# Kernel tuning notes

Measured on AMD Instinct MI355X. Metric: run time of the kernel, lower is better.

## Reference

```python
import jax, jax.numpy as jnp
import numpy as np
import math

K = 8  # n_prototypes
SQRT_2_OVER_PI = 0.7978845608028654  # sqrt(2/pi)
EPS = 1e-12  # torch F.normalize eps


def _gelu(x):
    # tanh-approx GELU, matching the module's _gelu
    return 0.5 * x * (1.0 + jnp.tanh(SQRT_2_OVER_PI * (x + 0.044715 * x * x * x)))


def _l2norm(x, axis=-1):
    n = jnp.linalg.norm(x, axis=axis, keepdims=True)
    return x / jnp.maximum(n, EPS)


def setup_inputs() -> dict:
    key = jax.random.key(0)
    k1, k2 = jax.random.split(key)
    B, T, D = 8, 2048, 2048
    x = jax.random.normal(k1, (B, T, D), dtype=jnp.float32)
    # prototype bank as it exists after initialization: unit-norm rows
    protos = _l2norm(jax.random.normal(k2, (K, D), dtype=jnp.float32))
    log_tau = jnp.asarray(math.log(2.0), dtype=jnp.float32)
    log_gamma = jnp.asarray(math.log(2.0), dtype=jnp.float32)
    log_blend = jnp.asarray(math.log(0.3 / 0.7), dtype=jnp.float32)
    return {"x": x, "protos": protos, "log_tau": log_tau,
            "log_gamma": log_gamma, "log_blend": log_blend}


def reference(x, protos, log_tau, log_gamma, log_blend):
    # steady-state (self._ready == True) forward path
    tau = jnp.exp(log_tau)
    gamma = jnp.exp(log_gamma)
    alpha = jax.nn.sigmoid(log_blend)

    out = _gelu(x)                                  # [B,T,D]
    out_norm = _l2norm(out)                         # [B,T,D]
    proto_norm = _l2norm(protos)                    # [K,D]
    sims = jnp.einsum('btd,kd->btk', out_norm, proto_norm)  # [B,T,K]
    soft_max_sim = (jax.nn.logsumexp(sims * tau, axis=-1) / tau
                    - jnp.log(jnp.float32(K)) / tau)         # [B,T]
    novelty = jnp.exp(-gamma * soft_max_sim)
    gate = 1.0 - alpha + alpha * novelty            # [B,T]
    return out * gate[..., None]
```

## Files before the change

### kernel.cpp

```cpp
#include <hip/hip_runtime.h>
#include <math.h>

#define DDIM 2048
#define KP 8
#define BLOCK 256

typedef float f4 __attribute__((ext_vector_type(4)));

#if __has_builtin(__builtin_amdgcn_fdot2_f32_bf16)
#define HAVE_DOT2 1
typedef __bf16 bf2 __attribute__((ext_vector_type(2)));
#else
#define HAVE_DOT2 0
#endif

#if __has_builtin(__builtin_amdgcn_update_dpp)
#define HAVE_DPP 1
#else
#define HAVE_DPP 0
#endif

__device__ __forceinline__ unsigned short f32_to_bf16_rne(float f) {
    unsigned u = __float_as_uint(f);
    unsigned r = u + 0x7FFFu + ((u >> 16) & 1u);
    return (unsigned short)(r >> 16);
}

__device__ __forceinline__ f4 gelu_f4(f4 x) {
    f4 x2 = x * x;
    f4 inner = x * (x2 * 0.044715f + 1.0f);
    f4 t = inner * -1.5957691216057308f;
    f4 e;
    e.x = __expf(t.x); e.y = __expf(t.y);
    e.z = __expf(t.z); e.w = __expf(t.w);
    f4 den = e + 1.0f;
    f4 r;
    r.x = __builtin_amdgcn_rcpf(den.x); r.y = __builtin_amdgcn_rcpf(den.y);
    r.z = __builtin_amdgcn_rcpf(den.z); r.w = __builtin_amdgcn_rcpf(den.w);
    return x * r;
}

__device__ __forceinline__ float wave_reduce_add(float v) {
#pragma unroll
    for (int m = 32; m >= 1; m >>= 1) v += __shfl_xor(v, m, 64);
    return v;
}

#if HAVE_DPP
template <int CTRL>
__device__ __forceinline__ float dpp_add(float v) {
    int t = __builtin_amdgcn_update_dpp(0, __builtin_bit_cast(int, v),
                                        CTRL, 0xf, 0xf, true);
    return v + __builtin_bit_cast(float, t);
}
__device__ __forceinline__ float wave_sum_dpp_lane63(float v) {
    v = dpp_add<0x111>(v);
    v = dpp_add<0x112>(v);
    v = dpp_add<0x114>(v);
    v = dpp_add<0x118>(v);
    v = dpp_add<0x142>(v);
    v = dpp_add<0x143>(v);
    return v;
}
#endif

__global__ void proto_prep_kernel(const float* __restrict__ protos,
                                  unsigned short* __restrict__ pb,
                                  float* __restrict__ inv_pn) {
    const int k = blockIdx.x;
    const int tid = threadIdx.x;
    const float* p = protos + k * DDIM;
    float ss = 0.0f;
#pragma unroll
    for (int i = 0; i < 2; ++i) {
        int idx = tid + i * 256;
        f4 a = reinterpret_cast<const f4*>(p)[idx];
        ushort4 u;
        u.x = f32_to_bf16_rne(a.x); u.y = f32_to_bf16_rne(a.y);
        u.z = f32_to_bf16_rne(a.z); u.w = f32_to_bf16_rne(a.w);
        float q;
        q = __uint_as_float((unsigned)u.x << 16); ss += q * q;
        q = __uint_as_float((unsigned)u.y << 16); ss += q * q;
        q = __uint_as_float((unsigned)u.z << 16); ss += q * q;
        q = __uint_as_float((unsigned)u.w << 16); ss += q * q;
        *reinterpret_cast<ushort4*>(&pb[(size_t)k * DDIM + idx * 4]) = u;
    }
    ss = wave_reduce_add(ss);
    __shared__ float red[4];
    const int wave = tid >> 6, lane = tid & 63;
    if (lane == 0) red[wave] = ss;
    __syncthreads();
    if (tid == 0)
        inv_pn[k] = 1.0f / fmaxf(sqrtf(red[0] + red[1] + red[2] + red[3]), 1e-12f);
}

__global__ __launch_bounds__(BLOCK)
void fused_row_kernel(const float* __restrict__ x,
                      const unsigned short* __restrict__ pb,
                      const float* __restrict__ lt,
                      const float* __restrict__ lg,
                      const float* __restrict__ lb,
                      const float* __restrict__ inv_pn,
                      float* __restrict__ out, int nrows) {
    alignas(16) __shared__ float red[2][18][4];

    const int tid = threadIdx.x;
    const int lane = tid & 63;
    const int wave = tid >> 6;

    const float tau = __expf(lt[0]);
    const float gamma = __expf(lg[0]);
    const float alpha = 1.0f / (1.0f + __expf(-lb[0]));
    const float inv_tau = 1.0f / tau;
    const float logK_div_tau = logf(8.0f) * inv_tau;

    float ipn[KP];
#pragma unroll
    for (int k = 0; k < KP; ++k) ipn[k] = inv_pn[k];

    const uint2* pb2 = reinterpret_cast<const uint2*>(pb);
    const int G = gridDim.x;

    int buf = 0;
    int r0 = blockIdx.x;
    if (r0 >= nrows) return;

    f4 a0, b0, a1, b1;
    {
        const int r1c = (r0 + G < nrows) ? r0 + G : r0;
        const f4* x0 = reinterpret_cast<const f4*>(x + (size_t)r0 * DDIM);
        const f4* x1 = reinterpret_cast<const f4*>(x + (size_t)r1c * DDIM);
        a0 = x0[tid]; b0 = x0[tid + 256];
        a1 = x1[tid]; b1 = x1[tid + 256];
    }

    for (; r0 < nrows; r0 += 2 * G) {
        const int r1 = r0 + G;
        const bool has1 = r1 < nrows;

        f4 g0a = gelu_f4(a0);
        f4 g0b = gelu_f4(b0);
        f4 g1a = gelu_f4(a1);
        f4 g1b = gelu_f4(b1);

        {
            const int n0 = r0 + 2 * G;
            if (n0 < nrows) {
                const int n1 = n0 + G;
                const int n1c = (n1 < nrows) ? n1 : n0;
                const f4* xn0 = reinterpret_cast<const f4*>(x + (size_t)n0 * DDIM);
                const f4* xn1 = reinterpret_cast<const f4*>(x + (size_t)n1c * DDIM);
                a0 = xn0[tid]; b0 = xn0[tid + 256];
                a1 = xn1[tid]; b1 = xn1[tid + 256];
            }
        }

        float vals[18];
        {
            f4 s0 = g0a * g0a + g0b * g0b;
            f4 s1 = g1a * g1a + g1b * g1b;
            vals[8] = (s0.x + s0.y) + (s0.z + s0.w);
            vals[17] = (s1.x + s1.y) + (s1.z + s1.w);
        }

#if HAVE_DOT2
        bf2 p0a, p0b, p0c, p0d, p1a, p1b, p1c, p1d;
        p0a.x = (__bf16)g0a.x; p0a.y = (__bf16)g0a.y;
        p0b.x = (__bf16)g0a.z; p0b.y = (__bf16)g0a.w;
        p0c.x = (__bf16)g0b.x; p0c.y = (__bf16)g0b.y;
        p0d.x = (__bf16)g0b.z; p0d.y = (__bf16)g0b.w;
        p1a.x = (__bf16)g1a.x; p1a.y = (__bf16)g1a.y;
        p1b.x = (__bf16)g1a.z; p1b.y = (__bf16)g1a.w;
        p1c.x = (__bf16)g1b.x; p1c.y = (__bf16)g1b.y;
        p1d.x = (__bf16)g1b.z; p1d.y = (__bf16)g1b.w;
#pragma unroll
        for (int k = 0; k < KP; ++k) {
            uint2 q0 = pb2[k * 512 + tid];
            uint2 q1 = pb2[k * 512 + 256 + tid];
            float t0, t1;
            t0 = __builtin_amdgcn_fdot2_f32_bf16(p0a, __builtin_bit_cast(bf2, q0.x), 0.0f, false);
            t1 = __builtin_amdgcn_fdot2_f32_bf16(p1a, __builtin_bit_cast(bf2, q0.x), 0.0f, false);
            t0 = __builtin_amdgcn_fdot2_f32_bf16(p0b, __builtin_bit_cast(bf2, q0.y), t0, false);
            t1 = __builtin_amdgcn_fdot2_f32_bf16(p1b, __builtin_bit_cast(bf2, q0.y), t1, false);
            t0 = __builtin_amdgcn_fdot2_f32_bf16(p0c, __builtin_bit_cast(bf2, q1.x), t0, false);
            t1 = __builtin_amdgcn_fdot2_f32_bf16(p1c, __builtin_bit_cast(bf2, q1.x), t1, false);
            t0 = __builtin_amdgcn_fdot2_f32_bf16(p0d, __builtin_bit_cast(bf2, q1.y), t0, false);
            t1 = __builtin_amdgcn_fdot2_f32_bf16(p1d, __builtin_bit_cast(bf2, q1.y), t1, false);
            vals[k] = t0;
            vals[9 + k] = t1;
        }
#else
#pragma unroll
        for (int k = 0; k < KP; ++k) {
            uint2 q0 = pb2[k * 512 + tid];
            uint2 q1 = pb2[k * 512 + 256 + tid];
            float c0 = __uint_as_float(q0.x << 16);
            float c1 = __uint_as_float(q0.x & 0xFFFF0000u);
            float c2 = __uint_as_float(q0.y << 16);
            float c3 = __uint_as_float(q0.y & 0xFFFF0000u);
            float c4 = __uint_as_float(q1.x << 16);
            float c5 = __uint_as_float(q1.x & 0xFFFF0000u);
            float c6 = __uint_as_float(q1.y << 16);
            float c7 = __uint_as_float(q1.y & 0xFFFF0000u);
            float t0, t1;
            t0 = fmaf(c0, g0a.x, c1 * g0a.y);
            t1 = fmaf(c0, g1a.x, c1 * g1a.y);
            t0 = fmaf(c2, g0a.z, t0); t0 = fmaf(c3, g0a.w, t0);
            t1 = fmaf(c2, g1a.z, t1); t1 = fmaf(c3, g1a.w, t1);
            t0 = fmaf(c4, g0b.x, t0); t0 = fmaf(c5, g0b.y, t0);
            t1 = fmaf(c4, g1b.x, t1); t1 = fmaf(c5, g1b.y, t1);
            t0 = fmaf(c6, g0b.z, t0); t0 = fmaf(c7, g0b.w, t0);
            t1 = fmaf(c6, g1b.z, t1); t1 = fmaf(c7, g1b.w, t1);
            vals[k] = t0;
            vals[9 + k] = t1;
        }
#endif

#if HAVE_DPP
#pragma unroll
        for (int v = 0; v < 18; ++v) vals[v] = wave_sum_dpp_lane63(vals[v]);
        if (lane == 63) {
#pragma unroll
            for (int v = 0; v < 18; ++v) red[buf][v][wave] = vals[v];
        }
#else
#pragma unroll
        for (int v = 0; v < 18; ++v) vals[v] = wave_reduce_add(vals[v]);
        if (lane == 0) {
#pragma unroll
            for (int v = 0; v < 18; ++v) red[buf][v][wave] = vals[v];
        }
#endif
        __syncthreads();

        float s[18];
#pragma unroll
        for (int v = 0; v < 18; ++v) {
            f4 r = *reinterpret_cast<const f4*>(red[buf][v]);
            s[v] = (r.x + r.y) + (r.z + r.w);
        }
        buf ^= 1;

        float gate0, gate1;
        {
            const float cn = __builtin_amdgcn_rcpf(fmaxf(sqrtf(s[8]), 1e-12f)) * tau;
            float e = 0.0f;
#pragma unroll
            for (int k = 0; k < KP; ++k)
                e += __expf(s[k] * ipn[k] * cn);
            float sms = __logf(e) * inv_tau - logK_div_tau;
            gate0 = 1.0f - alpha + alpha * __expf(-gamma * sms);
        }
        {
            const float cn = __builtin_amdgcn_rcpf(fmaxf(sqrtf(s[17]), 1e-12f)) * tau;
            float e = 0.0f;
#pragma unroll
            for (int k = 0; k < KP; ++k)
                e += __expf(s[9 + k] * ipn[k] * cn);
            float sms = __logf(e) * inv_tau - logK_div_tau;
            gate1 = 1.0f - alpha + alpha * __expf(-gamma * sms);
        }

        f4* o0 = reinterpret_cast<f4*>(out + (size_t)r0 * DDIM);
        f4 w0 = g0a * gate0;
        f4 w1 = g0b * gate0;
        __builtin_nontemporal_store(w0, &o0[tid]);
        __builtin_nontemporal_store(w1, &o0[tid + 256]);
        if (has1) {
            f4* o1 = reinterpret_cast<f4*>(out + (size_t)r1 * DDIM);
            f4 w2 = g1a * gate1;
            f4 w3 = g1b * gate1;
            __builtin_nontemporal_store(w2, &o1[tid]);
            __builtin_nontemporal_store(w3, &o1[tid + 256]);
        }
    }
}

extern "C" void kernel_launch(void* const* d_in, const int* in_sizes, int n_in,
                              void* d_out, int out_size, void* d_ws, size_t ws_size,
                              hipStream_t stream) {
    const float* x = (const float*)d_in[0];
    const float* protos = (const float*)d_in[1];
    const float* lt = (const float*)d_in[2];
    const float* lg = (const float*)d_in[3];
    const float* lb = (const float*)d_in[4];
    float* out = (float*)d_out;

    float* inv_pn = (float*)d_ws;
    unsigned short* pb = (unsigned short*)((char*)d_ws + 256);

    const int nrows = in_sizes[0] / DDIM;

    proto_prep_kernel<<<KP, 256, 0, stream>>>(protos, pb, inv_pn);

    int blocks = 2048;
    if (blocks > (nrows + 1) / 2) blocks = (nrows + 1) / 2;
    fused_row_kernel<<<blocks, BLOCK, 0, stream>>>(x, pb, lt, lg, lb, inv_pn,
                                                   out, nrows);
}
```

Measured before the change: 52.59 us.

## Replace persistent prefetching loop with one-block-per-row-pair launch

Drops the grid-stride persistent loop, which used software prefetch of the next row pair, and launches one block per pair of adjacent rows instead. Latency hiding now comes from more resident blocks rather than explicit double-buffering, and the shared reduction buffer shrinks to a single slot. In exchange, each block reloads the bf16 prototype bank and recomputes the scalar parameters, which raises L2 traffic and per-block setup cost.

```diff
diff --git a/kernel.cpp b/kernel.cpp
--- a/kernel.cpp
+++ b/kernel.cpp
@@ -95,18 +95,31 @@
 }
 
 __global__ __launch_bounds__(BLOCK)
-void fused_row_kernel(const float* __restrict__ x,
-                      const unsigned short* __restrict__ pb,
-                      const float* __restrict__ lt,
-                      const float* __restrict__ lg,
-                      const float* __restrict__ lb,
-                      const float* __restrict__ inv_pn,
-                      float* __restrict__ out, int nrows) {
-    alignas(16) __shared__ float red[2][18][4];
+void fused_pair_kernel(const float* __restrict__ x,
+                       const unsigned short* __restrict__ pb,
+                       const float* __restrict__ lt,
+                       const float* __restrict__ lg,
+                       const float* __restrict__ lb,
+                       const float* __restrict__ inv_pn,
+                       float* __restrict__ out, int nrows) {
+    alignas(16) __shared__ float red[18][4];
 
     const int tid = threadIdx.x;
     const int lane = tid & 63;
     const int wave = tid >> 6;
+
+    const int r0 = 2 * blockIdx.x;
+    const int r1 = r0 + 1;
+    if (r0 >= nrows) return;
+    const bool has1 = r1 < nrows;
+    const int r1c = has1 ? r1 : r0;
+
+    const f4* x0 = reinterpret_cast<const f4*>(x + (size_t)r0 * DDIM);
+    const f4* x1 = reinterpret_cast<const f4*>(x + (size_t)r1c * DDIM);
+    f4 a0 = x0[tid];
+    f4 b0 = x0[tid + 256];
+    f4 a1 = x1[tid];
+    f4 b1 = x1[tid + 256];
 
     const float tau = __expf(lt[0]);
     const float gamma = __expf(lg[0]);
@@ -119,160 +132,128 @@
     for (int k = 0; k < KP; ++k) ipn[k] = inv_pn[k];
 
     const uint2* pb2 = reinterpret_cast<const uint2*>(pb);
-    const int G = gridDim.x;
-
-    int buf = 0;
-    int r0 = blockIdx.x;
-    if (r0 >= nrows) return;
-
-    f4 a0, b0, a1, b1;
+
+    f4 g0a = gelu_f4(a0);
+    f4 g0b = gelu_f4(b0);
+    f4 g1a = gelu_f4(a1);
+    f4 g1b = gelu_f4(b1);
+
+    float vals[18];
     {
-        const int r1c = (r0 + G < nrows) ? r0 + G : r0;
-        const f4* x0 = reinterpret_cast<const f4*>(x + (size_t)r0 * DDIM);
-        const f4* x1 = reinterpret_cast<const f4*>(x + (size_t)r1c * DDIM);
-        a0 = x0[tid]; b0 = x0[tid + 256];
-        a1 = x1[tid]; b1 = x1[tid + 256];
-    }
-
-    for (; r0 < nrows; r0 += 2 * G) {
-        const int r1 = r0 + G;
-        const bool has1 = r1 < nrows;
-
-        f4 g0a = gelu_f4(a0);
-        f4 g0b = gelu_f4(b0);
-        f4 g1a = gelu_f4(a1);
-        f4 g1b = gelu_f4(b1);
-
-        {
-            const int n0 = r0 + 2 * G;
-            if (n0 < nrows) {
-                const int n1 = n0 + G;
-                const int n1c = (n1 < nrows) ? n1 : n0;
-                const f4* xn0 = reinterpret_cast<const f4*>(x + (size_t)n0 * DDIM);
-                const f4* xn1 = reinterpret_cast<const f4*>(x + (size_t)n1c * DDIM);
-                a0 = xn0[tid]; b0 = xn0[tid + 256];
-                a1 = xn1[tid]; b1 = xn1[tid + 256];
-            }
-        }
-
-        float vals[18];
-        {
-            f4 s0 = g0a * g0a + g0b * g0b;
-            f4 s1 = g1a * g1a + g1b * g1b;
-            vals[8] = (s0.x + s0.y) + (s0.z + s0.w);
-            vals[17] = (s1.x + s1.y) + (s1.z + s1.w);
-        }
+        f4 s0 = g0a * g0a + g0b * g0b;
+        f4 s1 = g1a * g1a + g1b * g1b;
+        vals[8] = (s0.x + s0.y) + (s0.z + s0.w);
+        vals[17] = (s1.x + s1.y) + (s1.z + s1.w);
+    }
 
 #if HAVE_DOT2
-        bf2 p0a, p0b, p0c, p0d, p1a, p1b, p1c, p1d;
-        p0a.x = (__bf16)g0a.x; p0a.y = (__bf16)g0a.y;
-        p0b.x = (__bf16)g0a.z; p0b.y = (__bf16)g0a.w;
-        p0c.x = (__bf16)g0b.x; p0c.y = (__bf16)g0b.y;
-        p0d.x = (__bf16)g0b.z; p0d.y = (__bf16)g0b.w;
-        p1a.x = (__bf16)g1a.x; p1a.y = (__bf16)g1a.y;
-        p1b.x = (__bf16)g1a.z; p1b.y = (__bf16)g1a.w;
-        p1c.x = (__bf16)g1b.x; p1c.y = (__bf16)g1b.y;
-        p1d.x = (__bf16)g1b.z; p1d.y = (__bf16)g1b.w;
-#pragma unroll
-        for (int k = 0; k < KP; ++k) {
-            uint2 q0 = pb2[k * 512 + tid];
-            uint2 q1 = pb2[k * 512 + 256 + tid];
-            float t0, t1;
-            t0 = __builtin_amdgcn_fdot2_f32_bf16(p0a, __builtin_bit_cast(bf2, q0.x), 0.0f, false);
-            t1 = __builtin_amdgcn_fdot2_f32_bf16(p1a, __builtin_bit_cast(bf2, q0.x), 0.0f, false);
-            t0 = __builtin_amdgcn_fdot2_f32_bf16(p0b, __builtin_bit_cast(bf2, q0.y), t0, false);
-            t1 = __builtin_amdgcn_fdot2_f32_bf16(p1b, __builtin_bit_cast(bf2, q0.y), t1, false);
-            t0 = __builtin_amdgcn_fdot2_f32_bf16(p0c, __builtin_bit_cast(bf2, q1.x), t0, false);
-            t1 = __builtin_amdgcn_fdot2_f32_bf16(p1c, __builtin_bit_cast(bf2, q1.x), t1, false);
-            t0 = __builtin_amdgcn_fdot2_f32_bf16(p0d, __builtin_bit_cast(bf2, q1.y), t0, false);
-            t1 = __builtin_amdgcn_fdot2_f32_bf16(p1d, __builtin_bit_cast(bf2, q1.y), t1, false);
-            vals[k] = t0;
-            vals[9 + k] = t1;
-        }
-#else
-#pragma unroll
-        for (int k = 0; k < KP; ++k) {
-            uint2 q0 = pb2[k * 512 + tid];
-            uint2 q1 = pb2[k * 512 + 256 + tid];
-            float c0 = __uint_as_float(q0.x << 16);
-            float c1 = __uint_as_float(q0.x & 0xFFFF0000u);
-            float c2 = __uint_as_float(q0.y << 16);
-            float c3 = __uint_as_float(q0.y & 0xFFFF0000u);
-            float c4 = __uint_as_float(q1.x << 16);
-            float c5 = __uint_as_float(q1.x & 0xFFFF0000u);
-            float c6 = __uint_as_float(q1.y << 16);
-            float c7 = __uint_as_float(q1.y & 0xFFFF0000u);
-            float t0, t1;
-            t0 = fmaf(c0, g0a.x, c1 * g0a.y);
-            t1 = fmaf(c0, g1a.x, c1 * g1a.y);
-            t0 = fmaf(c2, g0a.z, t0); t0 = fmaf(c3, g0a.w, t0);
-            t1 = fmaf(c2, g1a.z, t1); t1 = fmaf(c3, g1a.w, t1);
-            t0 = fmaf(c4, g0b.x, t0); t0 = fmaf(c5, g0b.y, t0);
-            t1 = fmaf(c4, g1b.x, t1); t1 = fmaf(c5, g1b.y, t1);
-            t0 = fmaf(c6, g0b.z, t0); t0 = fmaf(c7, g0b.w, t0);
-            t1 = fmaf(c6, g1b.z, t1); t1 = fmaf(c7, g1b.w, t1);
-            vals[k] = t0;
-            vals[9 + k] = t1;
-        }
+    bf2 p0a, p0b, p0c, p0d, p1a, p1b, p1c, p1d;
+    p0a.x = (__bf16)g0a.x; p0a.y = (__bf16)g0a.y;
+    p0b.x = (__bf16)g0a.z; p0b.y = (__bf16)g0a.w;
+    p0c.x = (__bf16)g0b.x; p0c.y = (__bf16)g0b.y;
+    p0d.x = (__bf16)g0b.z; p0d.y = (__bf16)g0b.w;
+    p1a.x = (__bf16)g1a.x; p1a.y = (__bf16)g1a.y;
+    p1b.x = (__bf16)g1a.z; p1b.y = (__bf16)g1a.w;
+    p1c.x = (__bf16)g1b.x; p1c.y = (__bf16)g1b.y;
+    p1d.x = (__bf16)g1b.z; p1d.y = (__bf16)g1b.w;
+#pragma unroll
+    for (int k = 0; k < KP; ++k) {
+        uint2 q0 = pb2[k * 512 + tid];
+        uint2 q1 = pb2[k * 512 + 256 + tid];
+        float t0, t1;
+        t0 = __builtin_amdgcn_fdot2_f32_bf16(p0a, __builtin_bit_cast(bf2, q0.x), 0.0f, false);
+        t1 = __builtin_amdgcn_fdot2_f32_bf16(p1a, __builtin_bit_cast(bf2, q0.x), 0.0f, false);
+        t0 = __builtin_amdgcn_fdot2_f32_bf16(p0b, __builtin_bit_cast(bf2, q0.y), t0, false);
+        t1 = __builtin_amdgcn_fdot2_f32_bf16(p1b, __builtin_bit_cast(bf2, q0.y), t1, false);
+        t0 = __builtin_amdgcn_fdot2_f32_bf16(p0c, __builtin_bit_cast(bf2, q1.x), t0, false);
+        t1 = __builtin_amdgcn_fdot2_f32_bf16(p1c, __builtin_bit_cast(bf2, q1.x), t1, false);
+        t0 = __builtin_amdgcn_fdot2_f32_bf16(p0d, __builtin_bit_cast(bf2, q1.y), t0, false);
+        t1 = __builtin_amdgcn_fdot2_f32_bf16(p1d, __builtin_bit_cast(bf2, q1.y), t1, false);
+        vals[k] = t0;
+        vals[9 + k] = t1;
+    }
+#else
+#pragma unroll
+    for (int k = 0; k < KP; ++k) {
+        uint2 q0 = pb2[k * 512 + tid];
+        uint2 q1 = pb2[k * 512 + 256 + tid];
+        float c0 = __uint_as_float(q0.x << 16);
+        float c1 = __uint_as_float(q0.x & 0xFFFF0000u);
+        float c2 = __uint_as_float(q0.y << 16);
+        float c3 = __uint_as_float(q0.y & 0xFFFF0000u);
+        float c4 = __uint_as_float(q1.x << 16);
+        float c5 = __uint_as_float(q1.x & 0xFFFF0000u);
+        float c6 = __uint_as_float(q1.y << 16);
+        float c7 = __uint_as_float(q1.y & 0xFFFF0000u);
+        float t0, t1;
+        t0 = fmaf(c0, g0a.x, c1 * g0a.y);
+        t1 = fmaf(c0, g1a.x, c1 * g1a.y);
+        t0 = fmaf(c2, g0a.z, t0); t0 = fmaf(c3, g0a.w, t0);
+        t1 = fmaf(c2, g1a.z, t1); t1 = fmaf(c3, g1a.w, t1);
+        t0 = fmaf(c4, g0b.x, t0); t0 = fmaf(c5, g0b.y, t0);
+        t1 = fmaf(c4, g1b.x, t1); t1 = fmaf(c5, g1b.y, t1);
+        t0 = fmaf(c6, g0b.z, t0); t0 = fmaf(c7, g0b.w, t0);
+        t1 = fmaf(c6, g1b.z, t1); t1 = fmaf(c7, g1b.w, t1);
+        vals[k] = t0;
+        vals[9 + k] = t1;
+    }
 #endif
 
 #if HAVE_DPP
 #pragma unroll
-        for (int v = 0; v < 18; ++v) vals[v] = wave_sum_dpp_lane63(vals[v]);
-        if (lane == 63) {
-#pragma unroll
-            for (int v = 0; v < 18; ++v) red[buf][v][wave] = vals[v];
-        }
-#else
-#pragma unroll
-        for (int v = 0; v < 18; ++v) vals[v] = wave_reduce_add(vals[v]);
-        if (lane == 0) {
-#pragma unroll
-            for (int v = 0; v < 18; ++v) red[buf][v][wave] = vals[v];
-        }
-#endif
-        __syncthreads();
-
-        float s[18];
-#pragma unroll
-        for (int v = 0; v < 18; ++v) {
-            f4 r = *reinterpret_cast<const f4*>(red[buf][v]);
-            s[v] = (r.x + r.y) + (r.z + r.w);
-        }
-        buf ^= 1;
-
-        float gate0, gate1;
-        {
-            const float cn = __builtin_amdgcn_rcpf(fmaxf(sqrtf(s[8]), 1e-12f)) * tau;
-            float e = 0.0f;
-#pragma unroll
-            for (int k = 0; k < KP; ++k)
-                e += __expf(s[k] * ipn[k] * cn);
-            float sms = __logf(e) * inv_tau - logK_div_tau;
-            gate0 = 1.0f - alpha + alpha * __expf(-gamma * sms);
-        }
-        {
-            const float cn = __builtin_amdgcn_rcpf(fmaxf(sqrtf(s[17]), 1e-12f)) * tau;
-            float e = 0.0f;
-#pragma unroll
-            for (int k = 0; k < KP; ++k)
-                e += __expf(s[9 + k] * ipn[k] * cn);
-            float sms = __logf(e) * inv_tau - logK_div_tau;
-            gate1 = 1.0f - alpha + alpha * __expf(-gamma * sms);
-        }
-
-        f4* o0 = reinterpret_cast<f4*>(out + (size_t)r0 * DDIM);
-        f4 w0 = g0a * gate0;
-        f4 w1 = g0b * gate0;
-        __builtin_nontemporal_store(w0, &o0[tid]);
-        __builtin_nontemporal_store(w1, &o0[tid + 256]);
-        if (has1) {
-            f4* o1 = reinterpret_cast<f4*>(out + (size_t)r1 * DDIM);
-            f4 w2 = g1a * gate1;
-            f4 w3 = g1b * gate1;
-            __builtin_nontemporal_store(w2, &o1[tid]);
-            __builtin_nontemporal_store(w3, &o1[tid + 256]);
-        }
+    for (int v = 0; v < 18; ++v) vals[v] = wave_sum_dpp_lane63(vals[v]);
+    if (lane == 63) {
+#pragma unroll
+        for (int v = 0; v < 18; ++v) red[v][wave] = vals[v];
+    }
+#else
+#pragma unroll
+    for (int v = 0; v < 18; ++v) vals[v] = wave_reduce_add(vals[v]);
+    if (lane == 0) {
+#pragma unroll
+        for (int v = 0; v < 18; ++v) red[v][wave] = vals[v];
+    }
+#endif
+    __syncthreads();
+
+    float s[18];
+#pragma unroll
+    for (int v = 0; v < 18; ++v) {
+        f4 r = *reinterpret_cast<const f4*>(red[v]);
+        s[v] = (r.x + r.y) + (r.z + r.w);
+    }
+
+    float gate0, gate1;
+    {
+        const float cn = __builtin_amdgcn_rcpf(fmaxf(sqrtf(s[8]), 1e-12f)) * tau;
+        float e = 0.0f;
+#pragma unroll
+        for (int k = 0; k < KP; ++k)
+            e += __expf(s[k] * ipn[k] * cn);
+        float sms = __logf(e) * inv_tau - logK_div_tau;
+        gate0 = 1.0f - alpha + alpha * __expf(-gamma * sms);
+    }
+    {
+        const float cn = __builtin_amdgcn_rcpf(fmaxf(sqrtf(s[17]), 1e-12f)) * tau;
+        float e = 0.0f;
+#pragma unroll
+        for (int k = 0; k < KP; ++k)
+            e += __expf(s[9 + k] * ipn[k] * cn);
+        float sms = __logf(e) * inv_tau - logK_div_tau;
+        gate1 = 1.0f - alpha + alpha * __expf(-gamma * sms);
+    }
+
+    f4* o0 = reinterpret_cast<f4*>(out + (size_t)r0 * DDIM);
+    f4 w0 = g0a * gate0;
+    f4 w1 = g0b * gate0;
+    __builtin_nontemporal_store(w0, &o0[tid]);
+    __builtin_nontemporal_store(w1, &o0[tid + 256]);
+    if (has1) {
+        f4* o1 = reinterpret_cast<f4*>(out + (size_t)r1 * DDIM);
+        f4 w2 = g1a * gate1;
+        f4 w3 = g1b * gate1;
+        __builtin_nontemporal_store(w2, &o1[tid]);
+        __builtin_nontemporal_store(w3, &o1[tid + 256]);
     }
 }
 
@@ -293,8 +274,7 @@
 
     proto_prep_kernel<<<KP, 256, 0, stream>>>(protos, pb, inv_pn);
 
-    int blocks = 2048;
-    if (blocks > (nrows + 1) / 2) blocks = (nrows + 1) / 2;
-    fused_row_kernel<<<blocks, BLOCK, 0, stream>>>(x, pb, lt, lg, lb, inv_pn,
-                                                   out, nrows);
-}
+    const int blocks = (nrows + 1) / 2;
+    fused_pair_kernel<<<blocks, BLOCK, 0, stream>>>(x, pb, lt, lg, lb, inv_pn,
+                                                    out, nrows);
+}
```

New measurement: 51.28 us. 1.03x faster.
